# Kernel optimization log

Measured on AMD Instinct MI355X. Metric: run time of the kernel, lower is better.

Reference implementation:

```python
import jax, jax.numpy as jnp
import numpy as np

N_HEADS = 16

def setup_inputs() -> dict:
    key = jax.random.key(0)
    k0, k1, k2 = jax.random.split(key, 3)
    B, T, C = 4, 2048, 1024
    x = jax.random.normal(k0, (B, T, C), dtype=jnp.float32)
    # nn.Linear params: y = x @ W.T + b
    w_qkv = jax.random.normal(k1, (3 * C, C), dtype=jnp.float32) * 0.02
    b_qkv = jnp.zeros((3 * C,), dtype=jnp.float32)
    w_proj = jax.random.normal(k2, (C, C), dtype=jnp.float32) * 0.02
    b_proj = jnp.zeros((C,), dtype=jnp.float32)
    return {"x": x, "w_qkv": w_qkv, "b_qkv": b_qkv, "w_proj": w_proj, "b_proj": b_proj}

def reference(x, w_qkv, b_qkv, w_proj, b_proj):
    B, T, C = x.shape
    H = N_HEADS
    hd = C // H
    qkv = x @ w_qkv.T + b_qkv                      # [B, T, 3C]
    q, k, v = jnp.split(qkv, 3, axis=-1)           # each [B, T, C]
    q = q.reshape(B, T, H, hd).transpose(0, 2, 1, 3)  # [B, H, T, hd]
    k = k.reshape(B, T, H, hd).transpose(0, 2, 1, 3)
    v = v.reshape(B, T, H, hd).transpose(0, 2, 1, 3)
    # note: original scales by emb_dim**-0.5 (C), not head_dim**-0.5
    wei = jnp.einsum("bhqd,bhkd->bhqk", q, k) * (C ** -0.5)  # [B, H, T, T]
    causal = jnp.tril(jnp.ones((T, T), dtype=bool))
    wei = jnp.where(causal, wei, -jnp.inf)
    att = jax.nn.softmax(wei, axis=-1)
    out = jnp.einsum("bhqk,bhkd->bhqd", att, v)    # [B, H, T, hd]
    out = out.transpose(0, 2, 1, 3).reshape(B, T, C)
    return out @ w_proj.T + b_proj
```

## Files before the change

### kernel.cpp

```cpp
#include <hip/hip_runtime.h>
#include <hip/hip_bf16.h>

typedef __bf16 bf16;
typedef __bf16 bf16x8 __attribute__((ext_vector_type(8)));
typedef __bf16 bf16x4 __attribute__((ext_vector_type(4)));
typedef float  f32x4  __attribute__((ext_vector_type(4)));

#define LDS_ASYNC16(g, l)                                            \
  __builtin_amdgcn_global_load_lds(                                  \
      (const __attribute__((address_space(1))) void*)(g),            \
      (__attribute__((address_space(3))) void*)(l), 16, 0, 0)

#define QSCALE 0.04508421995f

__global__ void cvt3_f32_bf16(const float* __restrict__ i0, bf16* __restrict__ o0, int n0,
                              const float* __restrict__ i1, bf16* __restrict__ o1, int n1,
                              const float* __restrict__ i2, bf16* __restrict__ o2, int n2) {
  int i = blockIdx.x * blockDim.x + threadIdx.x;
  const float* in;
  bf16* out;
  if (i < n0) {
    in = i0; out = o0;
  } else if (i < n0 + n1) {
    i -= n0; in = i1; out = o1;
  } else {
    i -= n0 + n1;
    if (i >= n2) return;
    in = i2; out = o2;
  }
  float4 v = ((const float4*)in)[i];
  bf16x4 o = {(bf16)v.x, (bf16)v.y, (bf16)v.z, (bf16)v.w};
  ((bf16x4*)out)[i] = o;
}

template <int MODE>
__global__ __launch_bounds__(256) void gemm_bt(
    const bf16* __restrict__ A, const bf16* __restrict__ B,
    const float* __restrict__ bias, float* __restrict__ outf,
    bf16* __restrict__ oq, bf16* __restrict__ ok, bf16* __restrict__ ov,
    int M, int N, int K) {
  __shared__ bf16 As[2][128 * 32];
  __shared__ bf16 Bs[2][128 * 32];
  const int tid = threadIdx.x;
  const int wave = tid >> 6, lane = tid & 63;
  const int quad = lane >> 4, l15 = lane & 15;
  const int bm = blockIdx.x * 128, bn = blockIdx.y * 128;
  const int wrow = (wave >> 1) << 6, wcol = (wave & 1) << 6;
  const int srow = tid >> 2;
  const int schunk = (tid & 3) * 8;

  f32x4 acc[4][4] = {};

  const bf16* ga0 = A + (size_t)(bm + srow) * K + schunk;
  const bf16* ga1 = A + (size_t)(bm + srow + 64) * K + schunk;
  const bf16* gb0 = B + (size_t)(bn + srow) * K + schunk;
  const bf16* gb1 = B + (size_t)(bn + srow + 64) * K + schunk;
  char* lA = (char*)As + wave * 1024;
  char* lB = (char*)Bs + wave * 1024;

  for (int k0 = 0; k0 < K; k0 += 64) {
    __syncthreads();
    LDS_ASYNC16(ga0 + k0, lA);
    LDS_ASYNC16(ga1 + k0, lA + 4096);
    LDS_ASYNC16(gb0 + k0, lB);
    LDS_ASYNC16(gb1 + k0, lB + 4096);
    LDS_ASYNC16(ga0 + k0 + 32, lA + 8192);
    LDS_ASYNC16(ga1 + k0 + 32, lA + 8192 + 4096);
    LDS_ASYNC16(gb0 + k0 + 32, lB + 8192);
    LDS_ASYNC16(gb1 + k0 + 32, lB + 8192 + 4096);
    __syncthreads();
#pragma unroll
    for (int s = 0; s < 2; ++s) {
      bf16x8 af[4], bfr[4];
#pragma unroll
      for (int mi = 0; mi < 4; ++mi)
        af[mi] = *(const bf16x8*)&As[s][(wrow + mi * 16 + l15) * 32 + quad * 8];
#pragma unroll
      for (int ni = 0; ni < 4; ++ni)
        bfr[ni] = *(const bf16x8*)&Bs[s][(wcol + ni * 16 + l15) * 32 + quad * 8];
#pragma unroll
      for (int mi = 0; mi < 4; ++mi)
#pragma unroll
        for (int ni = 0; ni < 4; ++ni)
          acc[mi][ni] = __builtin_amdgcn_mfma_f32_16x16x32_bf16(
              af[mi], bfr[ni], acc[mi][ni], 0, 0, 0);
    }
  }

#pragma unroll
  for (int mi = 0; mi < 4; ++mi) {
    const int row0 = bm + wrow + mi * 16 + quad * 4;
#pragma unroll
    for (int ni = 0; ni < 4; ++ni) {
      const int col = bn + wcol + ni * 16 + l15;
      const float bv = bias[col];
      if (MODE == 0) {
#pragma unroll
        for (int r = 0; r < 4; ++r)
          outf[(size_t)(row0 + r) * N + col] = acc[mi][ni][r] + bv;
      } else {
        const int part = col >> 10;
        const int cn = col & 1023, h = cn >> 6, d = cn & 63;
        const int b = row0 >> 11, t0 = row0 & 2047;
        if (part == 2) {
          bf16x4 pk = {(bf16)(acc[mi][ni][0] + bv), (bf16)(acc[mi][ni][1] + bv),
                       (bf16)(acc[mi][ni][2] + bv), (bf16)(acc[mi][ni][3] + bv)};
          *(bf16x4*)(ov + ((size_t)(b * 16 + h) * 64 + d) * 2048 + t0) = pk;
        } else {
          const float sc = part ? 1.0f : QSCALE;
          bf16* dst = (part ? ok : oq) + ((size_t)(b * 16 + h) * 2048 + t0) * 64 + d;
#pragma unroll
          for (int r = 0; r < 4; ++r)
            dst[(size_t)r * 64] = (bf16)((acc[mi][ni][r] + bv) * sc);
        }
      }
    }
  }
}

__global__ __launch_bounds__(256) void flash_attn(
    const bf16* __restrict__ qb, const bf16* __restrict__ kb,
    const bf16* __restrict__ vt, bf16* __restrict__ ob) {
  constexpr int T = 2048;
  __shared__ bf16 Ks[2][64 * 72];
  __shared__ bf16 Vs[2][64 * 72];
  __shared__ float Ls[4][2][4][16];
  const int tid = threadIdx.x, wave = tid >> 6, lane = tid & 63;
  const int quad = lane >> 4, l15 = lane & 15;
  const int bh = blockIdx.x;
  const int b = bh >> 4, h = bh & 15;
  const bf16* qbase = qb + (size_t)bh * T * 64;
  const bf16* kbase = kb + (size_t)bh * T * 64;
  const bf16* vbase = vt + (size_t)bh * 64 * T;
  const int srow = tid >> 3, sc = (tid & 7) * 8;

  const int vp0 = (sc & ~31) | ((sc & 8) << 1) | ((sc & 16) >> 2);

  const int qt = 15 - (int)blockIdx.y;
  const int q0 = qt * 128 + wave * 32;

  bf16x8 qf[2][2];
#pragma unroll
  for (int qi = 0; qi < 2; ++qi)
#pragma unroll
    for (int ks = 0; ks < 2; ++ks)
      qf[qi][ks] = *(const bf16x8*)(qbase + (size_t)(q0 + qi * 16 + l15) * 64 +
                                    ks * 32 + quad * 8);

  f32x4 lsumv[2] = {};
  f32x4 oacc[2][4] = {};

  const int nkt = 2 * qt + 2;
  const int ktp = q0 >> 6;

  {
    uint4 k0 = *(const uint4*)(kbase + (size_t)srow * 64 + sc);
    uint4 k1 = *(const uint4*)(kbase + (size_t)(srow + 32) * 64 + sc);
    uint4 v0 = *(const uint4*)(vbase + (size_t)srow * T + sc);
    uint4 v1 = *(const uint4*)(vbase + (size_t)(srow + 32) * T + sc);
    *(uint4*)&Ks[0][srow * 72 + sc] = k0;
    *(uint4*)&Ks[0][(srow + 32) * 72 + sc] = k1;
    *(uint2*)&Vs[0][srow * 72 + vp0] = make_uint2(v0.x, v0.y);
    *(uint2*)&Vs[0][srow * 72 + vp0 + 8] = make_uint2(v0.z, v0.w);
    *(uint2*)&Vs[0][(srow + 32) * 72 + vp0] = make_uint2(v1.x, v1.y);
    *(uint2*)&Vs[0][(srow + 32) * 72 + vp0 + 8] = make_uint2(v1.z, v1.w);
  }

#pragma unroll 1
  for (int kt = 0; kt < nkt; ++kt) {
    __syncthreads();
    const int cur = kt & 1;
    const bool pre = (kt + 1) < nkt;
    uint4 pk0, pk1, pv0, pv1;
    if (pre) {
      const bf16* kp = kbase + (size_t)(kt + 1) * 64 * 64;
      const bf16* vp = vbase + (kt + 1) * 64;
      pk0 = *(const uint4*)(kp + (size_t)srow * 64 + sc);
      pk1 = *(const uint4*)(kp + (size_t)(srow + 32) * 64 + sc);
      pv0 = *(const uint4*)(vp + (size_t)srow * T + sc);
      pv1 = *(const uint4*)(vp + (size_t)(srow + 32) * T + sc);
    }
    if (kt <= ktp) {
      f32x4 st[4][2];
      __builtin_amdgcn_s_setprio(1);
#pragma unroll
      for (int ki = 0; ki < 4; ++ki) {
        bf16x8 kfa = *(const bf16x8*)&Ks[cur][(ki * 16 + l15) * 72 + quad * 8];
        bf16x8 kfb =
            *(const bf16x8*)&Ks[cur][(ki * 16 + l15) * 72 + 32 + quad * 8];
#pragma unroll
        for (int qi = 0; qi < 2; ++qi) {
          f32x4 a = {0.f, 0.f, 0.f, 0.f};
          a = __builtin_amdgcn_mfma_f32_16x16x32_bf16(kfa, qf[qi][0], a, 0, 0, 0);
          a = __builtin_amdgcn_mfma_f32_16x16x32_bf16(kfb, qf[qi][1], a, 0, 0, 0);
          st[ki][qi] = a;
        }
      }
      __builtin_amdgcn_s_setprio(0);
      if (kt == ktp) {
#pragma unroll
        for (int ki = 0; ki < 4; ++ki)
#pragma unroll
          for (int qi = 0; qi < 2; ++qi)
#pragma unroll
            for (int r = 0; r < 4; ++r) {
              const int kcol = kt * 64 + ki * 16 + quad * 4 + r;
              const int qrow = q0 + qi * 16 + l15;
              if (kcol > qrow) st[ki][qi][r] = -__builtin_inff();
            }
      }
#pragma unroll
      for (int ki = 0; ki < 4; ++ki)
#pragma unroll
        for (int qi = 0; qi < 2; ++qi) {
#pragma unroll
          for (int r = 0; r < 4; ++r)
            st[ki][qi][r] = __builtin_amdgcn_exp2f(st[ki][qi][r]);
          lsumv[qi] += st[ki][qi];
        }
      bf16x8 pa8[2][2];
#pragma unroll
      for (int ki2 = 0; ki2 < 2; ++ki2)
#pragma unroll
        for (int qi = 0; qi < 2; ++qi) {
          bf16x8 p;
#pragma unroll
          for (int r = 0; r < 4; ++r) {
            p[r] = (bf16)st[2 * ki2][qi][r];
            p[r + 4] = (bf16)st[2 * ki2 + 1][qi][r];
          }
          pa8[ki2][qi] = p;
        }
      __builtin_amdgcn_s_setprio(1);
#pragma unroll
      for (int di = 0; di < 4; ++di)
#pragma unroll
        for (int ki2 = 0; ki2 < 2; ++ki2) {
          bf16x8 vv = *(const bf16x8*)&Vs[cur][(di * 16 + l15) * 72 + ki2 * 32 +
                                              quad * 8];
#pragma unroll
          for (int qi = 0; qi < 2; ++qi)
            oacc[qi][di] = __builtin_amdgcn_mfma_f32_16x16x32_bf16(
                pa8[ki2][qi], vv, oacc[qi][di], 0, 0, 0);
        }
      __builtin_amdgcn_s_setprio(0);
    }
    if (pre) {
      const int nxt = cur ^ 1;
      *(uint4*)&Ks[nxt][srow * 72 + sc] = pk0;
      *(uint4*)&Ks[nxt][(srow + 32) * 72 + sc] = pk1;
      *(uint2*)&Vs[nxt][srow * 72 + vp0] = make_uint2(pv0.x, pv0.y);
      *(uint2*)&Vs[nxt][srow * 72 + vp0 + 8] = make_uint2(pv0.z, pv0.w);
      *(uint2*)&Vs[nxt][(srow + 32) * 72 + vp0] = make_uint2(pv1.x, pv1.y);
      *(uint2*)&Vs[nxt][(srow + 32) * 72 + vp0 + 8] = make_uint2(pv1.z, pv1.w);
    }
  }

#pragma unroll
  for (int qi = 0; qi < 2; ++qi)
    Ls[wave][qi][quad][l15] =
        lsumv[qi][0] + lsumv[qi][1] + lsumv[qi][2] + lsumv[qi][3];
#pragma unroll
  for (int qi = 0; qi < 2; ++qi)
#pragma unroll
    for (int r = 0; r < 4; ++r) {
      const int rloc = quad * 4 + r;
      const float l = Ls[wave][qi][0][rloc] + Ls[wave][qi][1][rloc] +
                      Ls[wave][qi][2][rloc] + Ls[wave][qi][3][rloc];
      const float inv = 1.f / l;
      const int t = q0 + qi * 16 + rloc;
#pragma unroll
      for (int di = 0; di < 4; ++di) {
        const int d = di * 16 + l15;
        ob[((size_t)b * 2048 + t) * 1024 + h * 64 + d] =
            (bf16)(oacc[qi][di][r] * inv);
      }
    }
}

extern "C" void kernel_launch(void* const* d_in, const int* in_sizes, int n_in,
                              void* d_out, int out_size, void* d_ws,
                              size_t ws_size, hipStream_t stream) {
  const float* x = (const float*)d_in[0];
  const float* w_qkv = (const float*)d_in[1];
  const float* b_qkv = (const float*)d_in[2];
  const float* w_proj = (const float*)d_in[3];
  const float* b_proj = (const float*)d_in[4];
  float* out = (float*)d_out;

  const int B = 4, T = 2048, C = 1024;
  const size_t nx = (size_t)B * T * C;

  char* ws = (char*)d_ws;
  bf16* xb = (bf16*)ws;      ws += nx * 2;
  bf16* wqkvb = (bf16*)ws;   ws += (size_t)3 * C * C * 2;
  bf16* wprojb = (bf16*)ws;  ws += (size_t)C * C * 2;
  bf16* qb = (bf16*)ws;      ws += nx * 2;
  bf16* kbuf = (bf16*)ws;    ws += nx * 2;
  bf16* vtb = (bf16*)ws;     ws += nx * 2;
  bf16* attb = (bf16*)ws;    ws += nx * 2;

  const int n0 = (int)(nx / 4), n1 = 3 * C * C / 4, n2 = C * C / 4;
  cvt3_f32_bf16<<<(n0 + n1 + n2 + 255) / 256, 256, 0, stream>>>(
      x, xb, n0, w_qkv, wqkvb, n1, w_proj, wprojb, n2);

  dim3 g1(64, 24);
  gemm_bt<1><<<g1, 256, 0, stream>>>(xb, wqkvb, b_qkv, nullptr, qb, kbuf, vtb,
                                     B * T, 3 * C, C);
  dim3 g2(64, 16);
  flash_attn<<<g2, 256, 0, stream>>>(qb, kbuf, vtb, attb);

  dim3 g3(64, 8);
  gemm_bt<0><<<g3, 256, 0, stream>>>(attb, wprojb, b_proj, out, nullptr,
                                     nullptr, nullptr, B * T, C, C);
}
```

Measured before the change: 239.9 us.

## Restructure GEMM with 256x128 tiles, XOR-swizzled LDS and prefetch-ahead pipeline

The bf16 GEMM kernel now uses 512-thread blocks with 256x128 output tiles and K-step 64. The LDS layout is XOR-swizzled to avoid bank conflicts. Loads are double-buffered with explicit vmcnt waits so the next tile's global->LDS copy overlaps the MFMA work, and MFMA runs at raised priority via setprio. Each block needs more LDS (96KB), which may limit occupancy, and the grid is halved in the M direction.

Result: no change. 238.2 us (-0.7%).

```diff
diff --git a/kernel.cpp b/kernel.cpp
--- a/kernel.cpp
+++ b/kernel.cpp
@@ -34,58 +34,93 @@
 }
 
 template <int MODE>
-__global__ __launch_bounds__(256) void gemm_bt(
+__global__ __launch_bounds__(512, 2) void gemm_bt(
     const bf16* __restrict__ A, const bf16* __restrict__ B,
     const float* __restrict__ bias, float* __restrict__ outf,
     bf16* __restrict__ oq, bf16* __restrict__ ok, bf16* __restrict__ ov,
     int M, int N, int K) {
-  __shared__ bf16 As[2][128 * 32];
-  __shared__ bf16 Bs[2][128 * 32];
+  __shared__ __align__(16) bf16 As[2][256 * 64];
+  __shared__ __align__(16) bf16 Bs[2][128 * 64];
   const int tid = threadIdx.x;
   const int wave = tid >> 6, lane = tid & 63;
-  const int quad = lane >> 4, l15 = lane & 15;
-  const int bm = blockIdx.x * 128, bn = blockIdx.y * 128;
-  const int wrow = (wave >> 1) << 6, wcol = (wave & 1) << 6;
-  const int srow = tid >> 2;
-  const int schunk = (tid & 3) * 8;
+  const int quad = lane >> 4, l15 = lane & 15, l7 = l15 & 7;
+  const int bm = blockIdx.x * 256, bn = blockIdx.y * 128;
+  const int wrow = (wave >> 1) << 6;
+  const int wcol = (wave & 1) << 6;
 
   f32x4 acc[4][4] = {};
 
-  const bf16* ga0 = A + (size_t)(bm + srow) * K + schunk;
-  const bf16* ga1 = A + (size_t)(bm + srow + 64) * K + schunk;
-  const bf16* gb0 = B + (size_t)(bn + srow) * K + schunk;
-  const bf16* gb1 = B + (size_t)(bn + srow + 64) * K + schunk;
-  char* lA = (char*)As + wave * 1024;
-  char* lB = (char*)Bs + wave * 1024;
-
-  for (int k0 = 0; k0 < K; k0 += 64) {
-    __syncthreads();
-    LDS_ASYNC16(ga0 + k0, lA);
-    LDS_ASYNC16(ga1 + k0, lA + 4096);
-    LDS_ASYNC16(gb0 + k0, lB);
-    LDS_ASYNC16(gb1 + k0, lB + 4096);
-    LDS_ASYNC16(ga0 + k0 + 32, lA + 8192);
-    LDS_ASYNC16(ga1 + k0 + 32, lA + 8192 + 4096);
-    LDS_ASYNC16(gb0 + k0 + 32, lB + 8192);
-    LDS_ASYNC16(gb1 + k0 + 32, lB + 8192 + 4096);
-    __syncthreads();
-#pragma unroll
-    for (int s = 0; s < 2; ++s) {
-      bf16x8 af[4], bfr[4];
-#pragma unroll
-      for (int mi = 0; mi < 4; ++mi)
-        af[mi] = *(const bf16x8*)&As[s][(wrow + mi * 16 + l15) * 32 + quad * 8];
-#pragma unroll
-      for (int ni = 0; ni < 4; ++ni)
-        bfr[ni] = *(const bf16x8*)&Bs[s][(wcol + ni * 16 + l15) * 32 + quad * 8];
+  const int csw = ((tid & 7) ^ ((tid >> 3) & 7)) * 8;
+  const bf16* gA = A + (size_t)(bm + (tid >> 3)) * K + csw;
+  const bf16* gB = B + (size_t)(bn + (tid >> 3)) * K + csw;
+  const size_t K64 = (size_t)K * 64;
+  const int KT = K >> 6;
+
+#define STAGE_TILE(kti, cb) do {                                      \
+    const bf16* ak_ = gA + (size_t)(kti) * 64;                        \
+    const bf16* bk_ = gB + (size_t)(kti) * 64;                        \
+    char* la_ = (char*)As + (cb) * 32768 + wave * 1024;               \
+    char* lb_ = (char*)Bs + (cb) * 16384 + wave * 1024;               \
+    LDS_ASYNC16(ak_, la_);                                            \
+    LDS_ASYNC16(ak_ + K64, la_ + 8192);                               \
+    LDS_ASYNC16(ak_ + 2 * K64, la_ + 16384);                          \
+    LDS_ASYNC16(ak_ + 3 * K64, la_ + 24576);                          \
+    LDS_ASYNC16(bk_, lb_);                                            \
+    LDS_ASYNC16(bk_ + K64, lb_ + 8192);                               \
+  } while (0)
+
+  STAGE_TILE(0, 0);
+  STAGE_TILE(1, 1);
+
+#pragma unroll 1
+  for (int kt = 0; kt < KT; ++kt) {
+    const int c = kt & 1;
+    if (kt + 1 < KT)
+      asm volatile("s_waitcnt vmcnt(6)" ::: "memory");
+    else
+      asm volatile("s_waitcnt vmcnt(0)" ::: "memory");
+    __builtin_amdgcn_sched_barrier(0);
+    __builtin_amdgcn_s_barrier();
+    __builtin_amdgcn_sched_barrier(0);
+
+    bf16x8 af[4][2], bfr[4][2];
+    const char* baseA = (const char*)As + c * 32768;
+    const char* baseB = (const char*)Bs + c * 16384;
+#pragma unroll
+    for (int mi = 0; mi < 4; ++mi) {
+      const int row = wrow + mi * 16 + l15;
+#pragma unroll
+      for (int s = 0; s < 2; ++s)
+        af[mi][s] = *(const bf16x8*)(baseA + row * 128 +
+                                     (((s << 2) + quad) ^ l7) * 16);
+    }
+#pragma unroll
+    for (int ni = 0; ni < 4; ++ni) {
+      const int row = wcol + ni * 16 + l15;
+#pragma unroll
+      for (int s = 0; s < 2; ++s)
+        bfr[ni][s] = *(const bf16x8*)(baseB + row * 128 +
+                                      (((s << 2) + quad) ^ l7) * 16);
+    }
+    asm volatile("s_waitcnt lgkmcnt(0)" ::: "memory");
+    __builtin_amdgcn_sched_barrier(0);
+    __builtin_amdgcn_s_barrier();
+    __builtin_amdgcn_sched_barrier(0);
+
+    if (kt + 2 < KT) STAGE_TILE(kt + 2, c);
+
+    __builtin_amdgcn_s_setprio(1);
+#pragma unroll
+    for (int s = 0; s < 2; ++s)
 #pragma unroll
       for (int mi = 0; mi < 4; ++mi)
 #pragma unroll
         for (int ni = 0; ni < 4; ++ni)
           acc[mi][ni] = __builtin_amdgcn_mfma_f32_16x16x32_bf16(
-              af[mi], bfr[ni], acc[mi][ni], 0, 0, 0);
-    }
-  }
+              af[mi][s], bfr[ni][s], acc[mi][ni], 0, 0, 0);
+    __builtin_amdgcn_s_setprio(0);
+  }
+#undef STAGE_TILE
 
 #pragma unroll
   for (int mi = 0; mi < 4; ++mi) {
@@ -304,13 +339,13 @@
   cvt3_f32_bf16<<<(n0 + n1 + n2 + 255) / 256, 256, 0, stream>>>(
       x, xb, n0, w_qkv, wqkvb, n1, w_proj, wprojb, n2);
 
-  dim3 g1(64, 24);
-  gemm_bt<1><<<g1, 256, 0, stream>>>(xb, wqkvb, b_qkv, nullptr, qb, kbuf, vtb,
+  dim3 g1(32, 24);
+  gemm_bt<1><<<g1, 512, 0, stream>>>(xb, wqkvb, b_qkv, nullptr, qb, kbuf, vtb,
                                      B * T, 3 * C, C);
   dim3 g2(64, 16);
   flash_attn<<<g2, 256, 0, stream>>>(qb, kbuf, vtb, attb);
 
-  dim3 g3(64, 8);
-  gemm_bt<0><<<g3, 256, 0, stream>>>(attb, wprojb, b_proj, out, nullptr,
+  dim3 g3(32, 8);
+  gemm_bt<0><<<g3, 512, 0, stream>>>(attb, wprojb, b_proj, out, nullptr,
                                      nullptr, nullptr, B * T, C, C);
 }
```

## Software-pipeline GEMM loads with double-buffered async LDS and XOR swizzle

Applied to the files above, without the earlier changes.

The GEMM main loop is restructured. Before, each step synchronized twice around a single 64-wide K chunk and loaded it into two LDS halves. Now the loop is a two-stage pipeline over 32-wide K tiles: it issues async global-to-LDS loads for tile kt+2 while computing tile kt, and it waits with fine-grained vmcnt and barriers. LDS columns are XOR-swizzled to reduce bank conflicts, and the MFMA block runs under raised wave priority with launch_bounds occupancy 4. This is meant to hide global load latency and LDS conflicts, at the cost of more barriers per unit of K and reliance on hand-written waitcnt correctness.

Result: no change. 242.6 us (+1.1%).

```diff
diff --git a/kernel.cpp b/kernel.cpp
--- a/kernel.cpp
+++ b/kernel.cpp
@@ -34,58 +34,77 @@
 }
 
 template <int MODE>
-__global__ __launch_bounds__(256) void gemm_bt(
+__global__ __launch_bounds__(256, 4) void gemm_bt(
     const bf16* __restrict__ A, const bf16* __restrict__ B,
     const float* __restrict__ bias, float* __restrict__ outf,
     bf16* __restrict__ oq, bf16* __restrict__ ok, bf16* __restrict__ ov,
     int M, int N, int K) {
-  __shared__ bf16 As[2][128 * 32];
-  __shared__ bf16 Bs[2][128 * 32];
+  __shared__ __align__(16) bf16 As[2][128 * 32];
+  __shared__ __align__(16) bf16 Bs[2][128 * 32];
   const int tid = threadIdx.x;
   const int wave = tid >> 6, lane = tid & 63;
   const int quad = lane >> 4, l15 = lane & 15;
   const int bm = blockIdx.x * 128, bn = blockIdx.y * 128;
   const int wrow = (wave >> 1) << 6, wcol = (wave & 1) << 6;
-  const int srow = tid >> 2;
-  const int schunk = (tid & 3) * 8;
 
   f32x4 acc[4][4] = {};
 
-  const bf16* ga0 = A + (size_t)(bm + srow) * K + schunk;
-  const bf16* ga1 = A + (size_t)(bm + srow + 64) * K + schunk;
-  const bf16* gb0 = B + (size_t)(bn + srow) * K + schunk;
-  const bf16* gb1 = B + (size_t)(bn + srow + 64) * K + schunk;
+  const int csw = ((tid & 3) ^ ((tid >> 3) & 3)) * 8;
+  const bf16* gA = A + (size_t)(bm + (tid >> 2)) * K + csw;
+  const bf16* gB = B + (size_t)(bn + (tid >> 2)) * K + csw;
   char* lA = (char*)As + wave * 1024;
   char* lB = (char*)Bs + wave * 1024;
-
-  for (int k0 = 0; k0 < K; k0 += 64) {
-    __syncthreads();
-    LDS_ASYNC16(ga0 + k0, lA);
-    LDS_ASYNC16(ga1 + k0, lA + 4096);
-    LDS_ASYNC16(gb0 + k0, lB);
-    LDS_ASYNC16(gb1 + k0, lB + 4096);
-    LDS_ASYNC16(ga0 + k0 + 32, lA + 8192);
-    LDS_ASYNC16(ga1 + k0 + 32, lA + 8192 + 4096);
-    LDS_ASYNC16(gb0 + k0 + 32, lB + 8192);
-    LDS_ASYNC16(gb1 + k0 + 32, lB + 8192 + 4096);
-    __syncthreads();
-#pragma unroll
-    for (int s = 0; s < 2; ++s) {
-      bf16x8 af[4], bfr[4];
-#pragma unroll
-      for (int mi = 0; mi < 4; ++mi)
-        af[mi] = *(const bf16x8*)&As[s][(wrow + mi * 16 + l15) * 32 + quad * 8];
+  const size_t K64 = (size_t)K * 64;
+  const int KT = K >> 5;
+
+#define ST(kt, cb) do {                                   \
+    const bf16* a_ = gA + (size_t)(kt) * 32;              \
+    const bf16* b_ = gB + (size_t)(kt) * 32;              \
+    LDS_ASYNC16(a_, lA + (cb) * 8192);                    \
+    LDS_ASYNC16(a_ + K64, lA + (cb) * 8192 + 4096);       \
+    LDS_ASYNC16(b_, lB + (cb) * 8192);                    \
+    LDS_ASYNC16(b_ + K64, lB + (cb) * 8192 + 4096);       \
+  } while (0)
+
+  ST(0, 0);
+  ST(1, 1);
+  asm volatile("s_waitcnt vmcnt(4)" ::: "memory");
+  __builtin_amdgcn_s_barrier();
+
+  const int gsw = (quad ^ ((l15 >> 1) & 3)) * 16;
+
+#pragma unroll 1
+  for (int kt = 0; kt < KT; ++kt) {
+    const int c = kt & 1;
+    const char* bA = (const char*)As + c * 8192;
+    const char* bB = (const char*)Bs + c * 8192;
+    bf16x8 af[4], bfr[4];
+#pragma unroll
+    for (int mi = 0; mi < 4; ++mi)
+      af[mi] = *(const bf16x8*)(bA + (wrow + mi * 16 + l15) * 64 + gsw);
+#pragma unroll
+    for (int ni = 0; ni < 4; ++ni)
+      bfr[ni] = *(const bf16x8*)(bB + (wcol + ni * 16 + l15) * 64 + gsw);
+    asm volatile("s_waitcnt lgkmcnt(0)" ::: "memory");
+    __builtin_amdgcn_s_barrier();
+    if (kt + 2 < KT) ST(kt + 2, c);
+    __builtin_amdgcn_s_setprio(1);
+#pragma unroll
+    for (int mi = 0; mi < 4; ++mi)
 #pragma unroll
       for (int ni = 0; ni < 4; ++ni)
-        bfr[ni] = *(const bf16x8*)&Bs[s][(wcol + ni * 16 + l15) * 32 + quad * 8];
-#pragma unroll
-      for (int mi = 0; mi < 4; ++mi)
-#pragma unroll
-        for (int ni = 0; ni < 4; ++ni)
-          acc[mi][ni] = __builtin_amdgcn_mfma_f32_16x16x32_bf16(
-              af[mi], bfr[ni], acc[mi][ni], 0, 0, 0);
-    }
-  }
+        acc[mi][ni] = __builtin_amdgcn_mfma_f32_16x16x32_bf16(
+            af[mi], bfr[ni], acc[mi][ni], 0, 0, 0);
+    __builtin_amdgcn_s_setprio(0);
+    if (kt + 1 < KT) {
+      if (kt + 2 < KT)
+        asm volatile("s_waitcnt vmcnt(4)" ::: "memory");
+      else
+        asm volatile("s_waitcnt vmcnt(0)" ::: "memory");
+      __builtin_amdgcn_s_barrier();
+    }
+  }
+#undef ST
 
 #pragma unroll
   for (int mi = 0; mi < 4; ++mi) {
```
